# Kernel tuning notes

Hardware: AMD Instinct MI355X
Metric: run time of the kernel (lower is better)

Reference implementation:

```python
import jax, jax.numpy as jnp
import numpy as np

B, N, F_, H = 4, 2048, 1024, 16
DH = F_ // H
SCALE = F_ / 19.5  # module uses feats/19.5, not sqrt(head_dim)


def setup_inputs() -> dict:
    key = jax.random.key(0)
    ks = jax.random.split(key, 9)
    s = 1.0 / np.sqrt(F_)
    return {
        "x": jax.random.normal(ks[0], (B, N, F_), jnp.float32),
        "Wq": jax.random.normal(ks[1], (F_, F_), jnp.float32) * s,
        "bq": jax.random.normal(ks[2], (F_,), jnp.float32) * s,
        "Wk": jax.random.normal(ks[3], (F_, F_), jnp.float32) * s,
        "bk": jax.random.normal(ks[4], (F_,), jnp.float32) * s,
        "Wv": jax.random.normal(ks[5], (F_, F_), jnp.float32) * s,
        "bv": jax.random.normal(ks[6], (F_,), jnp.float32) * s,
        "Wo": jax.random.normal(ks[7], (F_, F_), jnp.float32) * s,
        "bo": jax.random.normal(ks[8], (F_,), jnp.float32) * s,
    }


def reference(x, Wq, bq, Wk, bk, Wv, bv, Wo, bo):
    b, n, f = x.shape
    # torch Linear: x @ W.T + b; then view(b,n,h,dh).transpose(1,2) -> bhnd
    def proj(W, bias):
        return (x @ W.T + bias).reshape(b, n, H, DH).transpose(0, 2, 1, 3)

    q = proj(Wq, bq)  # [b,h,n,dh]
    k = proj(Wk, bk)
    v = proj(Wv, bv)
    score = jax.nn.softmax(jnp.einsum("bhif,bhjf->bhij", q, k) / SCALE, axis=-1)
    attn = jnp.einsum("bhij,bhjf->bihf", score, v)  # [b,n,h,dh]
    o = attn.reshape(b, n, f) @ Wo.T + bo  # dropout p=0.0 -> identity
    return o
```

## Files before the change

kernel.cpp:

```cpp
#include <hip/hip_runtime.h>
#include <stdint.h>

typedef unsigned short u16;
typedef __bf16 bf16x8 __attribute__((ext_vector_type(8)));
typedef float f32x4 __attribute__((ext_vector_type(4)));

#define QSCALE (19.5f/1024.0f * 1.44269504088896340736f)

#define EXPB 16251.0f

__device__ __forceinline__ u16 f2bf(float f){
  uint32_t u = __float_as_uint(f);
  return (u16)((u + 0x7FFFu + ((u >> 16) & 1u)) >> 16);
}

__device__ __forceinline__ uint64_t cvt4(float4 f){
  union{ u16 u[4]; uint64_t v; } pk;
  pk.u[0]=f2bf(f.x); pk.u[1]=f2bf(f.y); pk.u[2]=f2bf(f.z); pk.u[3]=f2bf(f.w);
  return pk.v;
}

#define GLD_LDS16(g,l) __builtin_amdgcn_global_load_lds( \
    (const __attribute__((address_space(1))) void*)(g),  \
    (__attribute__((address_space(3))) void*)(l), 16, 0, 0)

__global__ __launch_bounds__(256) void k_prep(
    const float4* __restrict__ x,  const float4* __restrict__ Wq,
    const float4* __restrict__ Wk, const float4* __restrict__ Wv,
    const float4* __restrict__ Wo,
    const float4* __restrict__ bq, const float4* __restrict__ bk, const float4* __restrict__ bv,
    uint64_t* __restrict__ xb, uint64_t* __restrict__ wqkv, uint64_t* __restrict__ wob,
    float4* __restrict__ bqkv)
{
  const int NX = 2097152, NW = 262144;
  const int total = NX + 4*NW + 768;
  int i = blockIdx.x*256 + threadIdx.x;
  const int stride = gridDim.x*256;
  for (; i < total; i += stride){
    if (i < NX)             xb[i] = cvt4(x[i]);
    else if (i < NX+NW)     { int j = i-NX;      wqkv[j]      = cvt4(Wq[j]); }
    else if (i < NX+2*NW)   { int j = i-NX-NW;   wqkv[NW+j]   = cvt4(Wk[j]); }
    else if (i < NX+3*NW)   { int j = i-NX-2*NW; wqkv[2*NW+j] = cvt4(Wv[j]); }
    else if (i < NX+4*NW)   { int j = i-NX-3*NW; wob[j]       = cvt4(Wo[j]); }
    else {
      int j = i - NX - 4*NW;
      bqkv[j] = (j < 256) ? bq[j] : (j < 512 ? bk[j-256] : bv[j-512]);
    }
  }
}

template<int MODE>
__global__ __launch_bounds__(256) void gemm_bt(
    const u16* __restrict__ A, const u16* __restrict__ Bw,
    const float* __restrict__ bias, float* __restrict__ Cout,
    u16* __restrict__ q_ws, u16* __restrict__ k_ws, u16* __restrict__ v_ws)
{
  __shared__ u16 As[2][128*64];
  __shared__ u16 Bs[2][128*64];
  const int tid  = threadIdx.x;
  const int w    = tid >> 6, lane = tid & 63;
  const int wr   = w >> 1,  wc   = w & 1;
  const int g    = lane >> 4, c16 = lane & 15;
  const int nt   = blockIdx.x, mt = blockIdx.y;
  const size_t arow0 = (size_t)mt * 128, brow0 = (size_t)nt * 128;

  f32x4 acc[4][4] = {};

  const int s3 = lane >> 3;
  const int schunk = ((lane & 7) ^ s3) * 8;
  const u16* gA = A  + (arow0 + w*8 + s3)*1024 + schunk;
  const u16* gB = Bw + (brow0 + w*8 + s3)*1024 + schunk;

  auto stage = [&](int buf, int k0){
    #pragma unroll
    for (int i = 0; i < 4; i++){
      GLD_LDS16(gA + i*32768 + k0, &As[buf][i*2048 + w*512]);
      GLD_LDS16(gB + i*32768 + k0, &Bs[buf][i*2048 + w*512]);
    }
  };

  stage(0, 0);
  asm volatile("s_waitcnt vmcnt(0)" ::: "memory");
  __builtin_amdgcn_s_barrier();

  const int swz = (c16 & 7);
  int cur = 0;
  for (int t = 0; t < 16; t++){
    if (t < 15) stage(cur ^ 1, (t + 1) * 64);

    #pragma unroll
    for (int kc = 0; kc < 2; kc++){
      const int kchunk = ((kc*4 + g) ^ swz) * 8;
      bf16x8 af[4], bfr[4];
      #pragma unroll
      for (int m = 0; m < 4; m++)
        af[m]  = __builtin_bit_cast(bf16x8, *(const uint4*)(&As[cur][(wr*64 + m*16 + c16)*64 + kchunk]));
      #pragma unroll
      for (int n = 0; n < 4; n++)
        bfr[n] = __builtin_bit_cast(bf16x8, *(const uint4*)(&Bs[cur][(wc*64 + n*16 + c16)*64 + kchunk]));
      __builtin_amdgcn_s_setprio(1);
      #pragma unroll
      for (int m = 0; m < 4; m++)
        #pragma unroll
        for (int n = 0; n < 4; n++)
          acc[m][n] = __builtin_amdgcn_mfma_f32_16x16x32_bf16(af[m], bfr[n], acc[m][n], 0, 0, 0);
      __builtin_amdgcn_s_setprio(0);
    }

    if (t < 15){
      asm volatile("s_waitcnt vmcnt(0)" ::: "memory");
      __builtin_amdgcn_s_barrier();
      cur ^= 1;
    }
  }

  #pragma unroll
  for (int m = 0; m < 4; m++){
    const size_t i0 = arow0 + wr*64 + m*16 + g*4;
    #pragma unroll
    for (int n = 0; n < 4; n++){
      const int o = (int)brow0 + wc*64 + n*16 + c16;
      const float bias_v = bias[o];
      if (MODE == 0){
        const int proj = o >> 10, wi = o & 1023, hh = wi >> 6, dd = wi & 63;
        if (proj < 2){
          u16* base = (proj == 0) ? q_ws : k_ws;
          const float sc = (proj == 0) ? QSCALE : 1.0f;
          #pragma unroll
          for (int r = 0; r < 4; r++){
            const size_t i = i0 + r;
            const size_t bb = i >> 11, nn = i & 2047;
            base[((bb*16 + hh)*2048 + nn)*64 + dd] = f2bf((acc[m][n][r] + bias_v)*sc);
          }
        } else {
          const size_t bb = i0 >> 11, nn = i0 & 2047;
          union{ u16 u[4]; uint64_t v; } pk;
          #pragma unroll
          for (int r = 0; r < 4; r++) pk.u[r] = f2bf(acc[m][n][r] + bias_v);
          *reinterpret_cast<uint64_t*>(v_ws + ((bb*16 + hh)*64 + dd)*2048 + nn) = pk.v;
        }
      } else {
        #pragma unroll
        for (int r = 0; r < 4; r++)
          Cout[(i0 + r)*1024 + o] = acc[m][n][r] + bias_v;
      }
    }
  }
}

__global__ __launch_bounds__(256, 2) void attn_k(
    const u16* __restrict__ Q, const u16* __restrict__ Kb, const u16* __restrict__ Vt,
    u16* __restrict__ O)
{
  __shared__ u16 lds[3*8192];
  const int tid = threadIdx.x, w = tid >> 6, lane = tid & 63;
  const int g = lane >> 4, l16 = lane & 15;

  const int f   = ((blockIdx.x & 7) << 6) | (blockIdx.x >> 3);
  const int qt_ = f & 7, bh = f >> 3;
  const int b = bh >> 4, h = bh & 15;
  const size_t hb = (size_t)bh * 2048 * 64;

  const int qrow0 = qt_*256 + w*64 + l16;
  bf16x8 qf[4][2];
  #pragma unroll
  for (int qt = 0; qt < 4; qt++)
    #pragma unroll
    for (int kc = 0; kc < 2; kc++)
      qf[qt][kc] = __builtin_bit_cast(bf16x8,
        *(const uint4*)(Q + hb + (size_t)(qrow0 + qt*16)*64 + kc*32 + g*8));

  f32x4 acc[4][4] = {};
  f32x4 lacc[4] = {};

  union{ u16 u[8]; bf16x8 f; } one_;
  #pragma unroll
  for (int i = 0; i < 8; i++) one_.u[i] = 0x3F80;
  const bf16x8 onesv = one_.f;

  const int srowL = w*8 + (lane >> 3);
  const int schunk = ((lane & 7) ^ ((lane >> 3) & 7)) * 8;
  const u16* gKs = Kb + hb + (size_t)srowL*64   + schunk;
  const u16* gVs = Vt + hb + (size_t)srowL*2048 + schunk;

  u16* ldsK0 = &lds[w*512];
  u16* ldsV0 = &lds[4096 + w*512];

  const int kb0 = l16*64 + (g ^ (l16 & 7))*8;
  const int kb1 = kb0 ^ 32;
  const int vswz = l16 & 7, vlo = (g & 1)*4, vg2 = g >> 1;
  int vb[2][2];
  #pragma unroll
  for (int p = 0; p < 2; p++)
    #pragma unroll
    for (int pc = 0; pc < 2; pc++)
      vb[p][pc] = l16*64 + (((p*4 + pc*2 + vg2) ^ vswz) << 3) + vlo;

#define STAGE_T(B2) do{ \
    GLD_LDS16(gKs,          ldsK0 + (B2)*8192); \
    GLD_LDS16(gKs + 2048,   ldsK0 + (B2)*8192 + 2048); \
    GLD_LDS16(gVs,          ldsV0 + (B2)*8192); \
    GLD_LDS16(gVs + 65536,  ldsV0 + (B2)*8192 + 2048); \
    gKs += 4096; gVs += 64; \
  }while(0)

#define BODY_T(B, STG, VMW) do{ \
    if (STG) STAGE_T(((B)+2)%3); \
    _Pragma("unroll") \
    for (int p = 0; p < 2; p++){ \
      uint64_t pkk[2][4]; \
      _Pragma("unroll") \
      for (int jh = 0; jh < 2; jh++){ \
        const int jt = p*2 + jh; \
        bf16x8 kf0 = __builtin_bit_cast(bf16x8, *(const uint4*)(&lds[(B)*8192 + jt*1024] + kb0)); \
        bf16x8 kf1 = __builtin_bit_cast(bf16x8, *(const uint4*)(&lds[(B)*8192 + jt*1024] + kb1)); \
        _Pragma("unroll") \
        for (int qt = 0; qt < 4; qt++){ \
          f32x4 st = {0.f,0.f,0.f,0.f}; \
          st = __builtin_amdgcn_mfma_f32_16x16x32_bf16(kf0, qf[qt][0], st, 0, 0, 0); \
          st = __builtin_amdgcn_mfma_f32_16x16x32_bf16(kf1, qf[qt][1], st, 0, 0, 0); \
          const uint32_t e0 = (uint32_t)(int)fmaf(st[0], 128.f, EXPB); \
          const uint32_t e1 = (uint32_t)(int)fmaf(st[1], 128.f, EXPB); \
          const uint32_t e2 = (uint32_t)(int)fmaf(st[2], 128.f, EXPB); \
          const uint32_t e3 = (uint32_t)(int)fmaf(st[3], 128.f, EXPB); \
          pkk[jh][qt] = (uint64_t)(e0 & 0xFFFFu) | ((uint64_t)(e1 & 0xFFFFu) << 16) \
                      | ((uint64_t)(e2 & 0xFFFFu) << 32) | ((uint64_t)e3 << 48); \
        } \
      } \
      union { uint64_t v[2]; bf16x8 f; } pf[4]; \
      _Pragma("unroll") \
      for (int qt = 0; qt < 4; qt++){ pf[qt].v[0] = pkk[0][qt]; pf[qt].v[1] = pkk[1][qt]; } \
      __builtin_amdgcn_s_setprio(1); \
      _Pragma("unroll") \
      for (int qt = 0; qt < 4; qt++) \
        lacc[qt] = __builtin_amdgcn_mfma_f32_16x16x32_bf16(onesv, pf[qt].f, lacc[qt], 0, 0, 0); \
      _Pragma("unroll") \
      for (int dt = 0; dt < 4; dt++){ \
        union { uint64_t v[2]; bf16x8 f; } vf; \
        vf.v[0] = *(const uint64_t*)(&lds[(B)*8192 + 4096 + dt*1024] + vb[p][0]); \
        vf.v[1] = *(const uint64_t*)(&lds[(B)*8192 + 4096 + dt*1024] + vb[p][1]); \
        _Pragma("unroll") \
        for (int qt = 0; qt < 4; qt++) \
          acc[dt][qt] = __builtin_amdgcn_mfma_f32_16x16x32_bf16(vf.f, pf[qt].f, acc[dt][qt], 0, 0, 0); \
      } \
      __builtin_amdgcn_s_setprio(0); \
    } \
    if ((VMW) == 4){ asm volatile("s_waitcnt vmcnt(4)" ::: "memory"); __builtin_amdgcn_s_barrier(); } \
    else if ((VMW) == 0){ asm volatile("s_waitcnt vmcnt(0)" ::: "memory"); __builtin_amdgcn_s_barrier(); } \
  }while(0)

  STAGE_T(0); STAGE_T(1);
  asm volatile("s_waitcnt vmcnt(4)" ::: "memory");
  __builtin_amdgcn_s_barrier();

  #pragma unroll 1
  for (int rr = 0; rr < 10; rr++){
    BODY_T(0, 1, 4);
    BODY_T(1, 1, 4);
    BODY_T(2, 1, 4);
  }
  BODY_T(0, 0, 0);
  BODY_T(1, 0, -1);

#undef BODY_T
#undef STAGE_T

  float inv[4];
  #pragma unroll
  for (int qt = 0; qt < 4; qt++) inv[qt] = 1.f / lacc[qt][0];

  #pragma unroll
  for (int qt = 0; qt < 4; qt++){
    const size_t ob = (((size_t)(b*2048 + qrow0 + qt*16))*16 + h)*64;
    #pragma unroll
    for (int dt = 0; dt < 4; dt++){
      union{ u16 u[4]; uint64_t v; } pkk;
      #pragma unroll
      for (int r = 0; r < 4; r++) pkk.u[r] = f2bf(acc[dt][qt][r] * inv[qt]);
      *reinterpret_cast<uint64_t*>(O + ob + dt*16 + g*4) = pkk.v;
    }
  }
}

extern "C" void kernel_launch(void* const* d_in, const int* in_sizes, int n_in,
                              void* d_out, int out_size, void* d_ws, size_t ws_size,
                              hipStream_t stream)
{
  const float* x  = (const float*)d_in[0];
  const float* Wq = (const float*)d_in[1];
  const float* bq = (const float*)d_in[2];
  const float* Wk = (const float*)d_in[3];
  const float* bk = (const float*)d_in[4];
  const float* Wv = (const float*)d_in[5];
  const float* bv = (const float*)d_in[6];
  const float* Wo = (const float*)d_in[7];
  const float* bo = (const float*)d_in[8];
  float* out = (float*)d_out;

  char* ws = (char*)d_ws;
  size_t off = 0;
  auto bump = [&](size_t bytes){ size_t o = off; off = (off + bytes + 255) & ~(size_t)255; return o; };
  u16*  xb   = (u16*)  (ws + bump(8388608ull*2));
  u16*  wqkv = (u16*)  (ws + bump(3145728ull*2));
  u16*  wob  = (u16*)  (ws + bump(1048576ull*2));
  float* bqkv= (float*)(ws + bump(3072ull*4));
  u16*  qws  = (u16*)  (ws + bump(8388608ull*2));
  u16*  kws  = (u16*)  (ws + bump(8388608ull*2));
  u16*  vws  = (u16*)  (ws + bump(8388608ull*2));
  u16*  att  = (u16*)  (ws + bump(8388608ull*2));

  k_prep<<<2048, 256, 0, stream>>>(
      (const float4*)x, (const float4*)Wq, (const float4*)Wk, (const float4*)Wv, (const float4*)Wo,
      (const float4*)bq, (const float4*)bk, (const float4*)bv,
      (uint64_t*)xb, (uint64_t*)wqkv, (uint64_t*)wob, (float4*)bqkv);

  gemm_bt<0><<<dim3(24, 64), 256, 0, stream>>>(xb, wqkv, bqkv, nullptr, qws, kws, vws);
  attn_k<<<512, 256, 0, stream>>>(qws, kws, vws, att);
  gemm_bt<1><<<dim3(8, 64), 256, 0, stream>>>(att, wob, bo, out, nullptr, nullptr, nullptr);
}
```

Measured before the change: 170.3 us.

## Triple-buffer GEMM with BK=32 stages and partial vmcnt waits

```diff
diff --git a/kernel.cpp b/kernel.cpp
--- a/kernel.cpp
+++ b/kernel.cpp
@@ -55,8 +55,7 @@
     const float* __restrict__ bias, float* __restrict__ Cout,
     u16* __restrict__ q_ws, u16* __restrict__ k_ws, u16* __restrict__ v_ws)
 {
-  __shared__ u16 As[2][128*64];
-  __shared__ u16 Bs[2][128*64];
+  __shared__ u16 lds[3*8192];
   const int tid  = threadIdx.x;
   const int w    = tid >> 6, lane = tid & 63;
   const int wr   = w >> 1,  wc   = w & 1;
@@ -66,53 +65,61 @@
 
   f32x4 acc[4][4] = {};
 
-  const int s3 = lane >> 3;
-  const int schunk = ((lane & 7) ^ s3) * 8;
-  const u16* gA = A  + (arow0 + w*8 + s3)*1024 + schunk;
-  const u16* gB = Bw + (brow0 + w*8 + s3)*1024 + schunk;
-
-  auto stage = [&](int buf, int k0){
-    #pragma unroll
-    for (int i = 0; i < 4; i++){
-      GLD_LDS16(gA + i*32768 + k0, &As[buf][i*2048 + w*512]);
-      GLD_LDS16(gB + i*32768 + k0, &Bs[buf][i*2048 + w*512]);
-    }
-  };
-
-  stage(0, 0);
-  asm volatile("s_waitcnt vmcnt(0)" ::: "memory");
+  const int srow  = w*16 + (lane >> 2);
+  const int schk  = ((lane & 3) ^ ((lane >> 2) & 3)) * 8;
+  const u16* gA = A  + (arow0 + srow)*1024 + schk;
+  const u16* gB = Bw + (brow0 + srow)*1024 + schk;
+
+  u16* ldsA0 = &lds[w*512];
+  u16* ldsB0 = &lds[4096 + w*512];
+
+  const int rswz = (g ^ (c16 & 3)) * 8;
+  const int abase = (wr*64 + c16)*32 + rswz;
+  const int bbase = 4096 + (wc*64 + c16)*32 + rswz;
+
+#define GSTAGE(B2) do{ \
+    GLD_LDS16(gA,          ldsA0 + (B2)*8192); \
+    GLD_LDS16(gA + 65536,  ldsA0 + (B2)*8192 + 2048); \
+    GLD_LDS16(gB,          ldsB0 + (B2)*8192); \
+    GLD_LDS16(gB + 65536,  ldsB0 + (B2)*8192 + 2048); \
+    gA += 32; gB += 32; \
+  }while(0)
+
+#define GBODY(B, STG, VMW) do{ \
+    if (STG) GSTAGE(((B)+2)%3); \
+    bf16x8 af[4], bfr[4]; \
+    _Pragma("unroll") \
+    for (int m = 0; m < 4; m++) \
+      af[m]  = __builtin_bit_cast(bf16x8, *(const uint4*)(&lds[(B)*8192 + abase + m*512])); \
+    _Pragma("unroll") \
+    for (int n = 0; n < 4; n++) \
+      bfr[n] = __builtin_bit_cast(bf16x8, *(const uint4*)(&lds[(B)*8192 + bbase + n*512])); \
+    __builtin_amdgcn_s_setprio(1); \
+    _Pragma("unroll") \
+    for (int m = 0; m < 4; m++) \
+      _Pragma("unroll") \
+      for (int n = 0; n < 4; n++) \
+        acc[m][n] = __builtin_amdgcn_mfma_f32_16x16x32_bf16(af[m], bfr[n], acc[m][n], 0, 0, 0); \
+    __builtin_amdgcn_s_setprio(0); \
+    if ((VMW) == 4){ asm volatile("s_waitcnt vmcnt(4)" ::: "memory"); __builtin_amdgcn_s_barrier(); } \
+    else if ((VMW) == 0){ asm volatile("s_waitcnt vmcnt(0)" ::: "memory"); __builtin_amdgcn_s_barrier(); } \
+  }while(0)
+
+  GSTAGE(0); GSTAGE(1);
+  asm volatile("s_waitcnt vmcnt(4)" ::: "memory");
   __builtin_amdgcn_s_barrier();
 
-  const int swz = (c16 & 7);
-  int cur = 0;
-  for (int t = 0; t < 16; t++){
-    if (t < 15) stage(cur ^ 1, (t + 1) * 64);
-
-    #pragma unroll
-    for (int kc = 0; kc < 2; kc++){
-      const int kchunk = ((kc*4 + g) ^ swz) * 8;
-      bf16x8 af[4], bfr[4];
-      #pragma unroll
-      for (int m = 0; m < 4; m++)
-        af[m]  = __builtin_bit_cast(bf16x8, *(const uint4*)(&As[cur][(wr*64 + m*16 + c16)*64 + kchunk]));
-      #pragma unroll
-      for (int n = 0; n < 4; n++)
-        bfr[n] = __builtin_bit_cast(bf16x8, *(const uint4*)(&Bs[cur][(wc*64 + n*16 + c16)*64 + kchunk]));
-      __builtin_amdgcn_s_setprio(1);
-      #pragma unroll
-      for (int m = 0; m < 4; m++)
-        #pragma unroll
-        for (int n = 0; n < 4; n++)
-          acc[m][n] = __builtin_amdgcn_mfma_f32_16x16x32_bf16(af[m], bfr[n], acc[m][n], 0, 0, 0);
-      __builtin_amdgcn_s_setprio(0);
-    }
-
-    if (t < 15){
-      asm volatile("s_waitcnt vmcnt(0)" ::: "memory");
-      __builtin_amdgcn_s_barrier();
-      cur ^= 1;
-    }
-  }
+  #pragma unroll 1
+  for (int rr = 0; rr < 10; rr++){
+    GBODY(0, 1, 4);
+    GBODY(1, 1, 4);
+    GBODY(2, 1, 4);
+  }
+  GBODY(0, 0, 0);
+  GBODY(1, 0, -1);
+
+#undef GBODY
+#undef GSTAGE
 
   #pragma unroll
   for (int m = 0; m < 4; m++){
```

Result: no change. 169.7 us (-0.4%).
